# Optimization experiments

Measured on AMD Instinct MI355X. Metric: run time of the kernel, lower is better.

Reference implementation:

```python
import jax, jax.numpy as jnp
import numpy as np

TOP_K = 2  # matches init k


def setup_inputs() -> dict:
    key = jax.random.key(0)
    ks = jax.random.split(key, 5)
    B, S, D, E, H = 2, 2048, 1024, 8, 4096
    scale = 0.02
    return {
        "x": jax.random.normal(ks[0], (B, S, D), dtype=jnp.float32),
        "wg": jax.random.normal(ks[1], (D, E), dtype=jnp.float32) * scale,
        "w1": jax.random.normal(ks[2], (E, D, H), dtype=jnp.float32) * scale,
        "w3": jax.random.normal(ks[3], (E, D, H), dtype=jnp.float32) * scale,
        "w2": jax.random.normal(ks[4], (E, H, D), dtype=jnp.float32) * scale,
    }


def reference(x, wg, w1, w3, w2):
    # x: [B, S, D]; wg: [D, E]; w1/w3: [E, D, H]; w2: [E, H, D]
    B, S, D = x.shape
    E = wg.shape[1]
    T = B * S
    xt = x.reshape(T, D)

    # Top-k gating: softmax over expert logits, keep top-k, renormalize.
    logits = xt @ wg                                    # [T, E]
    probs = jax.nn.softmax(logits, axis=-1)             # [T, E]
    topv, topi = jax.lax.top_k(probs, TOP_K)            # [T, k]
    topv = topv / topv.sum(axis=-1, keepdims=True)
    # Dense combine weights [T, E] (zero for non-selected experts).
    comb = jnp.zeros((T, E), dtype=x.dtype).at[jnp.arange(T)[:, None], topi].set(topv)

    # Per-expert SwiGLU MLP with weighted combine (loop over small fixed E).
    out = jnp.zeros_like(xt)
    for e in range(E):
        h = jax.nn.silu(xt @ w1[e]) * (xt @ w3[e])      # [T, H]
        out = out + comb[:, e:e + 1] * (h @ w2[e])       # [T, D]
    return out.reshape(B, S, D)
```

## Files before the change

kernel.cpp:

```cpp
#include <hip/hip_runtime.h>
#include <cstdint>
#include <cstddef>

#define T_TOK 4096
#define DIM   1024
#define NEXP  8
#define HDIM  4096
#define NSLOT (2 * T_TOK)

#define BM 128
#define BN1 128
#define BN2 256
#define BK 32

typedef __attribute__((ext_vector_type(8))) short s16x8;
typedef __attribute__((ext_vector_type(4))) float f32x4;

__device__ __forceinline__ unsigned short f2bf(float f) {
    union { float f; unsigned u; } v; v.f = f;
    unsigned u = v.u;
    unsigned r = (u + 0x7FFFu + ((u >> 16) & 1u)) >> 16;
    return (unsigned short)r;
}

__device__ __forceinline__ int lds_off(int row, int kchunk) {
    return row * 32 + ((kchunk ^ ((row >> 1) & 3)) << 3);
}

__device__ __forceinline__ void gload16(const void* g, void* l) {
    __builtin_amdgcn_global_load_lds(
        (const __attribute__((address_space(1))) unsigned int*)g,
        (__attribute__((address_space(3))) unsigned int*)l, 16, 0, 0);
}

__global__ __launch_bounds__(256) void gate_kernel(
    const float* __restrict__ x, const float* __restrict__ wg,
    int* __restrict__ tok_e, float* __restrict__ tok_w, int* __restrict__ counts,
    unsigned short* __restrict__ xg)
{
    int t = blockIdx.x * 4 + (threadIdx.x >> 6);
    int lane = threadIdx.x & 63;
    float acc[NEXP];
#pragma unroll
    for (int e = 0; e < NEXP; ++e) acc[e] = 0.f;
    const float* xrow = x + (size_t)t * DIM;
    unsigned short* xgrow = xg + (size_t)t * DIM;
    for (int d = lane; d < DIM; d += 64) {
        float xv = xrow[d];
        xgrow[d] = f2bf(xv);
        const float4* wr = (const float4*)(wg + (size_t)d * NEXP);
        float4 w0 = wr[0], w1v = wr[1];
        acc[0] += xv * w0.x;  acc[1] += xv * w0.y;
        acc[2] += xv * w0.z;  acc[3] += xv * w0.w;
        acc[4] += xv * w1v.x; acc[5] += xv * w1v.y;
        acc[6] += xv * w1v.z; acc[7] += xv * w1v.w;
    }
#pragma unroll
    for (int e = 0; e < NEXP; ++e)
#pragma unroll
        for (int off = 32; off > 0; off >>= 1)
            acc[e] += __shfl_xor(acc[e], off);
    if (lane == 0) {
        int i0 = 0;
#pragma unroll
        for (int e = 1; e < NEXP; ++e) if (acc[e] > acc[i0]) i0 = e;
        int i1 = (i0 == 0) ? 1 : 0;
#pragma unroll
        for (int e = 0; e < NEXP; ++e) if (e != i0 && acc[e] > acc[i1]) i1 = e;
        float w0 = 1.f / (1.f + __expf(acc[i1] - acc[i0]));
        tok_e[2 * t] = i0;  tok_e[2 * t + 1] = i1;
        tok_w[2 * t] = w0;  tok_w[2 * t + 1] = 1.f - w0;
        atomicAdd(&counts[i0], 1);
        atomicAdd(&counts[i1], 1);
    }
}

__global__ void scan_kernel(const int* __restrict__ counts,
                            int* __restrict__ offsets, int* __restrict__ cursor)
{
    if (threadIdx.x == 0) {
        int s = 0;
        for (int e = 0; e < NEXP; ++e) { offsets[e] = s; s += counts[e]; cursor[e] = 0; }
        offsets[NEXP] = s;
    }
}

__global__ __launch_bounds__(256) void assign_kernel(
    const int* __restrict__ tok_e, const float* __restrict__ tok_w,
    const int* __restrict__ offsets, int* __restrict__ cursor,
    int* __restrict__ rows_tok, float* __restrict__ rows_gate)
{
    int t = blockIdx.x * 256 + threadIdx.x;
    if (t >= T_TOK) return;
#pragma unroll
    for (int j = 0; j < 2; ++j) {
        int e = tok_e[2 * t + j];
        int pos = offsets[e] + atomicAdd(&cursor[e], 1);
        rows_tok[pos] = t;
        rows_gate[pos] = tok_w[2 * t + j];
    }
}

__device__ __forceinline__ void tconv_body(
    const float* __restrict__ src, unsigned short* __restrict__ dst,
    int R, int C, int e, int bx, int by, int t)
{
    __shared__ unsigned int t_lds[64 * 33];
    int c0 = bx * 64, r0 = by * 64;
    int lane = t & 63, w = t >> 6;
    const float* s = src + (size_t)e * R * C + (size_t)(r0 + w * 16) * C + c0 + lane;
#pragma unroll
    for (int j = 0; j < 8; ++j) {
        float v0 = s[(size_t)(2 * j) * C];
        float v1 = s[(size_t)(2 * j + 1) * C];
        unsigned int pk = (unsigned int)f2bf(v0) | ((unsigned int)f2bf(v1) << 16);
        t_lds[lane * 33 + (w * 8 + j)] = pk;
    }
    __syncthreads();
    unsigned short* dbase = dst + (size_t)e * C * R;
#pragma unroll
    for (int rep = 0; rep < 2; ++rep) {
        int idx = rep * 256 + t;
        int c = idx >> 3, chunk = idx & 7;
        uint4 o;
        o.x = t_lds[c * 33 + chunk * 4 + 0];
        o.y = t_lds[c * 33 + chunk * 4 + 1];
        o.z = t_lds[c * 33 + chunk * 4 + 2];
        o.w = t_lds[c * 33 + chunk * 4 + 3];
        *(uint4*)(dbase + (size_t)(c0 + c) * R + r0 + chunk * 8) = o;
    }
}

__global__ __launch_bounds__(256) void tconv13_kernel(
    const float* __restrict__ w1, const float* __restrict__ w3,
    unsigned short* __restrict__ w1t, unsigned short* __restrict__ w3t)
{
    int z = blockIdx.z;
    if (z < NEXP)
        tconv_body(w1, w1t, DIM, HDIM, z, blockIdx.x, blockIdx.y, threadIdx.x);
    else
        tconv_body(w3, w3t, DIM, HDIM, z - NEXP, blockIdx.x, blockIdx.y, threadIdx.x);
}

__global__ __launch_bounds__(256) void tconv_kernel(
    const float* __restrict__ src, unsigned short* __restrict__ dst, int R, int C)
{
    tconv_body(src, dst, R, C, blockIdx.z, blockIdx.x, blockIdx.y, threadIdx.x);
}

__global__ __launch_bounds__(512, 4) void gemm1_kernel(
    const unsigned short* __restrict__ xg,
    const unsigned short* __restrict__ w1t, const unsigned short* __restrict__ w3t,
    const int* __restrict__ rows_tok, const int* __restrict__ offsets,
    unsigned short* __restrict__ h)
{
    int e = blockIdx.z;
    int offs = offsets[e];
    int cnt  = offsets[e + 1] - offs;
    int m0 = blockIdx.y * BM;
    if (m0 >= cnt) return;
    int n0 = blockIdx.x * BN1;

    __shared__ unsigned short lds3[3][3][BM * BK];
    __shared__ int toks[BM];

    int tid = threadIdx.x;
    if (tid < BM) toks[tid] = rows_tok[offs + min(m0 + tid, cnt - 1)];
    __syncthreads();

    int lane = tid & 63;
    int wid = tid >> 6;
    int wr = wid >> 2, wc = wid & 3;
    int lr = lane & 15, lg = lane >> 4;

    int srow = tid >> 2;
    int g = (tid & 3) ^ ((srow >> 1) & 3);
    const unsigned short* asrc  = xg  + (size_t)toks[srow] * DIM + g * 8;
    const unsigned short* b1src = w1t + ((size_t)e * HDIM + n0 + srow) * DIM + g * 8;
    const unsigned short* b3src = w3t + ((size_t)e * HDIM + n0 + srow) * DIM + g * 8;
    int ldsbase = wid * 512;

    f32x4 acc1[4][2] = {};
    f32x4 acc3[4][2] = {};

    const int NT = DIM / BK;

    auto stage_t = [&](int b, int t) {
        int k0 = t * BK;
        gload16(asrc + k0,  &lds3[b][0][ldsbase]);
        gload16(b1src + k0, &lds3[b][1][ldsbase]);
        gload16(b3src + k0, &lds3[b][2][ldsbase]);
    };

    stage_t(0, 0);
    stage_t(1, 1);

    int cur = 0;
    for (int t = 0; t < NT; ++t) {
        if (t == NT - 1) asm volatile("s_waitcnt vmcnt(0)" ::: "memory");
        else             asm volatile("s_waitcnt vmcnt(3)" ::: "memory");
        __builtin_amdgcn_s_barrier();

        int nxt = cur + 2; if (nxt >= 3) nxt -= 3;
        if (t + 2 < NT) stage_t(nxt, t + 2);

        s16x8 a[4], b1f[2], b3f[2];
#pragma unroll
        for (int m = 0; m < 4; ++m)
            a[m] = *(const s16x8*)&lds3[cur][0][lds_off(wr * 64 + m * 16 + lr, lg)];
#pragma unroll
        for (int n = 0; n < 2; ++n) {
            b1f[n] = *(const s16x8*)&lds3[cur][1][lds_off(wc * 32 + n * 16 + lr, lg)];
            b3f[n] = *(const s16x8*)&lds3[cur][2][lds_off(wc * 32 + n * 16 + lr, lg)];
        }

        __builtin_amdgcn_s_setprio(1);
#pragma unroll
        for (int n = 0; n < 2; ++n) {
#pragma unroll
            for (int m = 0; m < 4; ++m)
                acc1[m][n] = __builtin_amdgcn_mfma_f32_16x16x32_bf16(a[m], b1f[n], acc1[m][n], 0, 0, 0);
#pragma unroll
            for (int m = 0; m < 4; ++m)
                acc3[m][n] = __builtin_amdgcn_mfma_f32_16x16x32_bf16(a[m], b3f[n], acc3[m][n], 0, 0, 0);
        }
        __builtin_amdgcn_s_setprio(0);

        __builtin_amdgcn_s_barrier();
        cur = cur + 1; if (cur == 3) cur = 0;
    }

#pragma unroll
    for (int m = 0; m < 4; ++m)
#pragma unroll
        for (int n = 0; n < 2; ++n)
#pragma unroll
            for (int r = 0; r < 4; ++r) {
                int row_local = wr * 64 + m * 16 + lg * 4 + r;
                if (m0 + row_local < cnt) {
                    int col_local = wc * 32 + n * 16 + lr;
                    float g1 = acc1[m][n][r];
                    float hv = (g1 / (1.f + __expf(-g1))) * acc3[m][n][r];
                    h[(size_t)(offs + m0 + row_local) * HDIM + n0 + col_local] = f2bf(hv);
                }
            }
}

__global__ __launch_bounds__(512, 4) void gemm2_kernel(
    const unsigned short* __restrict__ h, const unsigned short* __restrict__ w2t,
    const int* __restrict__ rows_tok, const float* __restrict__ rows_gate,
    const int* __restrict__ offsets, float* __restrict__ out)
{
    int e = blockIdx.z;
    int offs = offsets[e];
    int cnt  = offsets[e + 1] - offs;
    int m0 = blockIdx.y * BM;
    if (m0 >= cnt) return;
    int n0 = blockIdx.x * BN2;

    __shared__ unsigned short ldsA[3][BM * BK];
    __shared__ unsigned short ldsB[3][BN2 * BK];
    __shared__ int   toks[BM];
    __shared__ float gts[BM];

    int tid = threadIdx.x;
    if (tid < BM) {
        int p = offs + min(m0 + tid, cnt - 1);
        toks[tid] = rows_tok[p];
        gts[tid]  = rows_gate[p];
    }
    __syncthreads();

    int lane = tid & 63;
    int wid = tid >> 6;
    int wr = wid >> 2, wc = wid & 3;
    int lr = lane & 15, lg = lane >> 4;

    int srow = tid >> 2;
    int g = (tid & 3) ^ ((srow >> 1) & 3);
    int arow = offs + min(m0 + srow, cnt - 1);
    const unsigned short* asrc  = h + (size_t)arow * HDIM + g * 8;
    const unsigned short* bsrc0 = w2t + ((size_t)e * DIM + n0 + srow) * HDIM + g * 8;
    const unsigned short* bsrc1 = w2t + ((size_t)e * DIM + n0 + 128 + srow) * HDIM + g * 8;
    int ldsbase = wid * 512;

    f32x4 acc[4][4] = {};

    const int NT = HDIM / BK;

    auto stage_t = [&](int b, int t) {
        int k0 = t * BK;
        gload16(asrc + k0,  &ldsA[b][ldsbase]);
        gload16(bsrc0 + k0, &ldsB[b][ldsbase]);
        gload16(bsrc1 + k0, &ldsB[b][4096 + ldsbase]);
    };

    stage_t(0, 0);
    stage_t(1, 1);

    int cur = 0;
    for (int t = 0; t < NT; ++t) {
        if (t == NT - 1) asm volatile("s_waitcnt vmcnt(0)" ::: "memory");
        else             asm volatile("s_waitcnt vmcnt(3)" ::: "memory");
        __builtin_amdgcn_s_barrier();

        int nxt = cur + 2; if (nxt >= 3) nxt -= 3;
        if (t + 2 < NT) stage_t(nxt, t + 2);

        s16x8 a[4], bf[4];
#pragma unroll
        for (int m = 0; m < 4; ++m)
            a[m] = *(const s16x8*)&ldsA[cur][lds_off(wr * 64 + m * 16 + lr, lg)];
#pragma unroll
        for (int n = 0; n < 4; ++n)
            bf[n] = *(const s16x8*)&ldsB[cur][lds_off(wc * 64 + n * 16 + lr, lg)];

        __builtin_amdgcn_s_setprio(1);
#pragma unroll
        for (int n = 0; n < 4; ++n)
#pragma unroll
            for (int m = 0; m < 4; ++m)
                acc[m][n] = __builtin_amdgcn_mfma_f32_16x16x32_bf16(a[m], bf[n], acc[m][n], 0, 0, 0);
        __builtin_amdgcn_s_setprio(0);

        __builtin_amdgcn_s_barrier();
        cur = cur + 1; if (cur == 3) cur = 0;
    }

#pragma unroll
    for (int m = 0; m < 4; ++m)
#pragma unroll
        for (int n = 0; n < 4; ++n)
#pragma unroll
            for (int r = 0; r < 4; ++r) {
                int row_local = wr * 64 + m * 16 + lg * 4 + r;
                if (m0 + row_local < cnt) {
                    int col = n0 + wc * 64 + n * 16 + lr;
                    float v = acc[m][n][r] * gts[row_local];
                    atomicAdd(&out[(size_t)toks[row_local] * DIM + col], v);
                }
            }
}

extern "C" void kernel_launch(void* const* d_in, const int* in_sizes, int n_in,
                              void* d_out, int out_size, void* d_ws, size_t ws_size,
                              hipStream_t stream)
{
    const float* x  = (const float*)d_in[0];
    const float* wg = (const float*)d_in[1];
    const float* w1 = (const float*)d_in[2];
    const float* w3 = (const float*)d_in[3];
    const float* w2 = (const float*)d_in[4];
    float* out = (float*)d_out;

    char* ws = (char*)d_ws;
    size_t off = 0;
    auto alloc = [&](size_t bytes) -> void* {
        void* p = ws + off;
        off = (off + bytes + 255) & ~(size_t)255;
        return p;
    };
    int*   rows_tok  = (int*)alloc((size_t)NSLOT * 4);
    float* rows_gate = (float*)alloc((size_t)NSLOT * 4);
    int*   tok_e     = (int*)alloc((size_t)NSLOT * 4);
    float* tok_w     = (float*)alloc((size_t)NSLOT * 4);
    int*   counts    = (int*)alloc(NEXP * 4);
    int*   offsets   = (int*)alloc((NEXP + 1) * 4);
    int*   cursor    = (int*)alloc(NEXP * 4);
    unsigned short* xg   = (unsigned short*)alloc((size_t)T_TOK * DIM * 2);
    unsigned short* w1t  = (unsigned short*)alloc((size_t)NEXP * HDIM * DIM * 2);
    unsigned short* w3t  = (unsigned short*)alloc((size_t)NEXP * HDIM * DIM * 2);
    unsigned short* hbuf = (unsigned short*)alloc((size_t)NSLOT * HDIM * 2);
    unsigned short* w2t  = w1t;

    hipMemsetAsync(counts, 0, NEXP * 4, stream);
    hipMemsetAsync(out, 0, (size_t)out_size * sizeof(float), stream);

    gate_kernel<<<T_TOK / 4, 256, 0, stream>>>(x, wg, tok_e, tok_w, counts, xg);
    scan_kernel<<<1, 64, 0, stream>>>(counts, offsets, cursor);
    assign_kernel<<<T_TOK / 256, 256, 0, stream>>>(tok_e, tok_w, offsets, cursor,
                                                   rows_tok, rows_gate);

    tconv13_kernel<<<dim3(HDIM / 64, DIM / 64, 2 * NEXP), 256, 0, stream>>>(
        w1, w3, w1t, w3t);

    gemm1_kernel<<<dim3(HDIM / BN1, T_TOK / BM, NEXP), 512, 0, stream>>>(
        xg, w1t, w3t, rows_tok, offsets, hbuf);

    tconv_kernel<<<dim3(DIM / 64, HDIM / 64, NEXP), 256, 0, stream>>>(w2, w2t, HDIM, DIM);

    gemm2_kernel<<<dim3(DIM / BN2, T_TOK / BM, NEXP), 512, 0, stream>>>(
        hbuf, w2t, rows_tok, rows_gate, offsets, out);
}
```

Measured before the change: 585.2 us.

## Interleave w1/w3 rows into one B matrix and pair gate/up via lane shuffle

The weight transpose kernel now writes w1 and w3 rows interleaved into a single buffer, so gemm1 loads one B tile instead of two. It keeps one accumulator set, and the SwiGLU pairing is done with a lane xor-shuffle in the epilogue. Columns per block are halved in effective output and the grid doubles in x. The cut in LDS and registers lets the launch bound occupancy rise from 4 to 6. In exchange, half the lanes are idle during the epilogue stores and the output writes become strided rather than contiguous.

```diff
diff --git a/kernel.cpp b/kernel.cpp
--- a/kernel.cpp
+++ b/kernel.cpp
@@ -131,15 +131,40 @@
     }
 }
 
-__global__ __launch_bounds__(256) void tconv13_kernel(
+__global__ __launch_bounds__(256) void tconv13i_kernel(
     const float* __restrict__ w1, const float* __restrict__ w3,
-    unsigned short* __restrict__ w1t, unsigned short* __restrict__ w3t)
-{
+    unsigned short* __restrict__ w13t)
+{
+    __shared__ unsigned int t_lds[64 * 33];
     int z = blockIdx.z;
-    if (z < NEXP)
-        tconv_body(w1, w1t, DIM, HDIM, z, blockIdx.x, blockIdx.y, threadIdx.x);
-    else
-        tconv_body(w3, w3t, DIM, HDIM, z - NEXP, blockIdx.x, blockIdx.y, threadIdx.x);
+    int parity = (z >= NEXP) ? 1 : 0;
+    int e = parity ? z - NEXP : z;
+    const float* src = parity ? w3 : w1;
+    const int R = DIM, C = HDIM;
+    int c0 = blockIdx.x * 64, r0 = blockIdx.y * 64;
+    int t = threadIdx.x;
+    int lane = t & 63, w = t >> 6;
+    const float* s = src + (size_t)e * R * C + (size_t)(r0 + w * 16) * C + c0 + lane;
+#pragma unroll
+    for (int j = 0; j < 8; ++j) {
+        float v0 = s[(size_t)(2 * j) * C];
+        float v1 = s[(size_t)(2 * j + 1) * C];
+        unsigned int pk = (unsigned int)f2bf(v0) | ((unsigned int)f2bf(v1) << 16);
+        t_lds[lane * 33 + (w * 8 + j)] = pk;
+    }
+    __syncthreads();
+    unsigned short* dbase = w13t + (size_t)e * 2 * C * R;
+#pragma unroll
+    for (int rep = 0; rep < 2; ++rep) {
+        int idx = rep * 256 + t;
+        int c = idx >> 3, chunk = idx & 7;
+        uint4 o;
+        o.x = t_lds[c * 33 + chunk * 4 + 0];
+        o.y = t_lds[c * 33 + chunk * 4 + 1];
+        o.z = t_lds[c * 33 + chunk * 4 + 2];
+        o.w = t_lds[c * 33 + chunk * 4 + 3];
+        *(uint4*)(dbase + (size_t)(2 * (c0 + c) + parity) * R + r0 + chunk * 8) = o;
+    }
 }
 
 __global__ __launch_bounds__(256) void tconv_kernel(
@@ -148,9 +173,9 @@
     tconv_body(src, dst, R, C, blockIdx.z, blockIdx.x, blockIdx.y, threadIdx.x);
 }
 
-__global__ __launch_bounds__(512, 4) void gemm1_kernel(
+__global__ __launch_bounds__(512, 6) void gemm1_kernel(
     const unsigned short* __restrict__ xg,
-    const unsigned short* __restrict__ w1t, const unsigned short* __restrict__ w3t,
+    const unsigned short* __restrict__ w13t,
     const int* __restrict__ rows_tok, const int* __restrict__ offsets,
     unsigned short* __restrict__ h)
 {
@@ -161,7 +186,7 @@
     if (m0 >= cnt) return;
     int n0 = blockIdx.x * BN1;
 
-    __shared__ unsigned short lds3[3][3][BM * BK];
+    __shared__ unsigned short lds3[3][2][BM * BK];
     __shared__ int toks[BM];
 
     int tid = threadIdx.x;
@@ -175,21 +200,18 @@
 
     int srow = tid >> 2;
     int g = (tid & 3) ^ ((srow >> 1) & 3);
-    const unsigned short* asrc  = xg  + (size_t)toks[srow] * DIM + g * 8;
-    const unsigned short* b1src = w1t + ((size_t)e * HDIM + n0 + srow) * DIM + g * 8;
-    const unsigned short* b3src = w3t + ((size_t)e * HDIM + n0 + srow) * DIM + g * 8;
+    const unsigned short* asrc = xg   + (size_t)toks[srow] * DIM + g * 8;
+    const unsigned short* bsrc = w13t + ((size_t)e * 2 * HDIM + n0 + srow) * DIM + g * 8;
     int ldsbase = wid * 512;
 
-    f32x4 acc1[4][2] = {};
-    f32x4 acc3[4][2] = {};
+    f32x4 acc[4][2] = {};
 
     const int NT = DIM / BK;
 
     auto stage_t = [&](int b, int t) {
         int k0 = t * BK;
-        gload16(asrc + k0,  &lds3[b][0][ldsbase]);
-        gload16(b1src + k0, &lds3[b][1][ldsbase]);
-        gload16(b3src + k0, &lds3[b][2][ldsbase]);
+        gload16(asrc + k0, &lds3[b][0][ldsbase]);
+        gload16(bsrc + k0, &lds3[b][1][ldsbase]);
     };
 
     stage_t(0, 0);
@@ -198,32 +220,26 @@
     int cur = 0;
     for (int t = 0; t < NT; ++t) {
         if (t == NT - 1) asm volatile("s_waitcnt vmcnt(0)" ::: "memory");
-        else             asm volatile("s_waitcnt vmcnt(3)" ::: "memory");
+        else             asm volatile("s_waitcnt vmcnt(2)" ::: "memory");
         __builtin_amdgcn_s_barrier();
 
         int nxt = cur + 2; if (nxt >= 3) nxt -= 3;
         if (t + 2 < NT) stage_t(nxt, t + 2);
 
-        s16x8 a[4], b1f[2], b3f[2];
+        s16x8 a[4], bf[2];
 #pragma unroll
         for (int m = 0; m < 4; ++m)
             a[m] = *(const s16x8*)&lds3[cur][0][lds_off(wr * 64 + m * 16 + lr, lg)];
 #pragma unroll
-        for (int n = 0; n < 2; ++n) {
-            b1f[n] = *(const s16x8*)&lds3[cur][1][lds_off(wc * 32 + n * 16 + lr, lg)];
-            b3f[n] = *(const s16x8*)&lds3[cur][2][lds_off(wc * 32 + n * 16 + lr, lg)];
-        }
+        for (int n = 0; n < 2; ++n)
+            bf[n] = *(const s16x8*)&lds3[cur][1][lds_off(wc * 32 + n * 16 + lr, lg)];
 
         __builtin_amdgcn_s_setprio(1);
 #pragma unroll
-        for (int n = 0; n < 2; ++n) {
+        for (int n = 0; n < 2; ++n)
 #pragma unroll
             for (int m = 0; m < 4; ++m)
-                acc1[m][n] = __builtin_amdgcn_mfma_f32_16x16x32_bf16(a[m], b1f[n], acc1[m][n], 0, 0, 0);
-#pragma unroll
-            for (int m = 0; m < 4; ++m)
-                acc3[m][n] = __builtin_amdgcn_mfma_f32_16x16x32_bf16(a[m], b3f[n], acc3[m][n], 0, 0, 0);
-        }
+                acc[m][n] = __builtin_amdgcn_mfma_f32_16x16x32_bf16(a[m], bf[n], acc[m][n], 0, 0, 0);
         __builtin_amdgcn_s_setprio(0);
 
         __builtin_amdgcn_s_barrier();
@@ -236,12 +252,14 @@
         for (int n = 0; n < 2; ++n)
 #pragma unroll
             for (int r = 0; r < 4; ++r) {
+                float g1 = acc[m][n][r];
+                float g3 = __shfl_xor(g1, 1);
                 int row_local = wr * 64 + m * 16 + lg * 4 + r;
-                if (m0 + row_local < cnt) {
-                    int col_local = wc * 32 + n * 16 + lr;
-                    float g1 = acc1[m][n][r];
-                    float hv = (g1 / (1.f + __expf(-g1))) * acc3[m][n][r];
-                    h[(size_t)(offs + m0 + row_local) * HDIM + n0 + col_local] = f2bf(hv);
+                if (((lane & 1) == 0) && (m0 + row_local < cnt)) {
+                    int gcol = n0 + wc * 32 + n * 16 + lr;
+                    int hcol = gcol >> 1;
+                    float hv = (g1 / (1.f + __expf(-g1))) * g3;
+                    h[(size_t)(offs + m0 + row_local) * HDIM + hcol] = f2bf(hv);
                 }
             }
 }
@@ -368,10 +386,9 @@
     int*   offsets   = (int*)alloc((NEXP + 1) * 4);
     int*   cursor    = (int*)alloc(NEXP * 4);
     unsigned short* xg   = (unsigned short*)alloc((size_t)T_TOK * DIM * 2);
-    unsigned short* w1t  = (unsigned short*)alloc((size_t)NEXP * HDIM * DIM * 2);
-    unsigned short* w3t  = (unsigned short*)alloc((size_t)NEXP * HDIM * DIM * 2);
+    unsigned short* w13t = (unsigned short*)alloc((size_t)NEXP * 2 * HDIM * DIM * 2);
     unsigned short* hbuf = (unsigned short*)alloc((size_t)NSLOT * HDIM * 2);
-    unsigned short* w2t  = w1t;
+    unsigned short* w2t  = w13t;
 
     hipMemsetAsync(counts, 0, NEXP * 4, stream);
     hipMemsetAsync(out, 0, (size_t)out_size * sizeof(float), stream);
@@ -381,11 +398,11 @@
     assign_kernel<<<T_TOK / 256, 256, 0, stream>>>(tok_e, tok_w, offsets, cursor,
                                                    rows_tok, rows_gate);
 
-    tconv13_kernel<<<dim3(HDIM / 64, DIM / 64, 2 * NEXP), 256, 0, stream>>>(
-        w1, w3, w1t, w3t);
-
-    gemm1_kernel<<<dim3(HDIM / BN1, T_TOK / BM, NEXP), 512, 0, stream>>>(
-        xg, w1t, w3t, rows_tok, offsets, hbuf);
+    tconv13i_kernel<<<dim3(HDIM / 64, DIM / 64, 2 * NEXP), 256, 0, stream>>>(
+        w1, w3, w13t);
+
+    gemm1_kernel<<<dim3(2 * HDIM / BN1, T_TOK / BM, NEXP), 512, 0, stream>>>(
+        xg, w13t, rows_tok, offsets, hbuf);
 
     tconv_kernel<<<dim3(DIM / 64, HDIM / 64, NEXP), 256, 0, stream>>>(w2, w2t, HDIM, DIM);
 
```

New measurement: 598.9 us. 1.02x slower.

## Load A operand directly from global into registers, shrink GEMM2 N tile

Applied to the files above, without the earlier changes.

Both grouped GEMMs stop staging the activation (A) tile through LDS. Each wave instead loads its A fragments straight from global memory into registers, double-buffered across even and odd k-steps, while only the weight tiles keep using the LDS triple buffer. GEMM2's N tile shrinks from 256 to 128, which halves its accumulators and doubles its grid. This removes LDS traffic and space for A and should raise occupancy, but adds uncoalesced per-lane global loads, duplicated A reads across the four waves that share rows, and extra reloads of the A rows in GEMM2.

```diff
diff --git a/kernel.cpp b/kernel.cpp
--- a/kernel.cpp
+++ b/kernel.cpp
@@ -10,7 +10,7 @@
 
 #define BM 128
 #define BN1 128
-#define BN2 256
+#define BN2 128
 #define BK 32
 
 typedef __attribute__((ext_vector_type(8))) short s16x8;
@@ -161,7 +161,7 @@
     if (m0 >= cnt) return;
     int n0 = blockIdx.x * BN1;
 
-    __shared__ unsigned short lds3[3][3][BM * BK];
+    __shared__ unsigned short lds3[3][2][BM * BK];
     __shared__ int toks[BM];
 
     int tid = threadIdx.x;
@@ -175,43 +175,46 @@
 
     int srow = tid >> 2;
     int g = (tid & 3) ^ ((srow >> 1) & 3);
-    const unsigned short* asrc  = xg  + (size_t)toks[srow] * DIM + g * 8;
     const unsigned short* b1src = w1t + ((size_t)e * HDIM + n0 + srow) * DIM + g * 8;
     const unsigned short* b3src = w3t + ((size_t)e * HDIM + n0 + srow) * DIM + g * 8;
     int ldsbase = wid * 512;
 
+    const unsigned short* abase[4];
+#pragma unroll
+    for (int m = 0; m < 4; ++m) {
+        int row = wr * 64 + m * 16 + lr;
+        abase[m] = xg + (size_t)toks[row] * DIM + lg * 8;
+    }
+
     f32x4 acc1[4][2] = {};
     f32x4 acc3[4][2] = {};
 
     const int NT = DIM / BK;
 
-    auto stage_t = [&](int b, int t) {
+    auto stageB = [&](int b, int t) {
         int k0 = t * BK;
-        gload16(asrc + k0,  &lds3[b][0][ldsbase]);
-        gload16(b1src + k0, &lds3[b][1][ldsbase]);
-        gload16(b3src + k0, &lds3[b][2][ldsbase]);
+        gload16(b1src + k0, &lds3[b][0][ldsbase]);
+        gload16(b3src + k0, &lds3[b][1][ldsbase]);
     };
 
-    stage_t(0, 0);
-    stage_t(1, 1);
-
-    int cur = 0;
-    for (int t = 0; t < NT; ++t) {
+    auto body = [&](int t, int cur, s16x8 (&au)[4], s16x8 (&ap)[4]) {
+        if (t + 1 < NT) {
+#pragma unroll
+            for (int m = 0; m < 4; ++m)
+                ap[m] = *(const s16x8*)(abase[m] + (t + 1) * BK);
+        }
         if (t == NT - 1) asm volatile("s_waitcnt vmcnt(0)" ::: "memory");
-        else             asm volatile("s_waitcnt vmcnt(3)" ::: "memory");
+        else             asm volatile("s_waitcnt vmcnt(6)" ::: "memory");
         __builtin_amdgcn_s_barrier();
 
         int nxt = cur + 2; if (nxt >= 3) nxt -= 3;
-        if (t + 2 < NT) stage_t(nxt, t + 2);
-
-        s16x8 a[4], b1f[2], b3f[2];
-#pragma unroll
-        for (int m = 0; m < 4; ++m)
-            a[m] = *(const s16x8*)&lds3[cur][0][lds_off(wr * 64 + m * 16 + lr, lg)];
+        if (t + 2 < NT) stageB(nxt, t + 2);
+
+        s16x8 b1f[2], b3f[2];
 #pragma unroll
         for (int n = 0; n < 2; ++n) {
-            b1f[n] = *(const s16x8*)&lds3[cur][1][lds_off(wc * 32 + n * 16 + lr, lg)];
-            b3f[n] = *(const s16x8*)&lds3[cur][2][lds_off(wc * 32 + n * 16 + lr, lg)];
+            b1f[n] = *(const s16x8*)&lds3[cur][0][lds_off(wc * 32 + n * 16 + lr, lg)];
+            b3f[n] = *(const s16x8*)&lds3[cur][1][lds_off(wc * 32 + n * 16 + lr, lg)];
         }
 
         __builtin_amdgcn_s_setprio(1);
@@ -219,15 +222,26 @@
         for (int n = 0; n < 2; ++n) {
 #pragma unroll
             for (int m = 0; m < 4; ++m)
-                acc1[m][n] = __builtin_amdgcn_mfma_f32_16x16x32_bf16(a[m], b1f[n], acc1[m][n], 0, 0, 0);
+                acc1[m][n] = __builtin_amdgcn_mfma_f32_16x16x32_bf16(au[m], b1f[n], acc1[m][n], 0, 0, 0);
 #pragma unroll
             for (int m = 0; m < 4; ++m)
-                acc3[m][n] = __builtin_amdgcn_mfma_f32_16x16x32_bf16(a[m], b3f[n], acc3[m][n], 0, 0, 0);
+                acc3[m][n] = __builtin_amdgcn_mfma_f32_16x16x32_bf16(au[m], b3f[n], acc3[m][n], 0, 0, 0);
         }
         __builtin_amdgcn_s_setprio(0);
-
         __builtin_amdgcn_s_barrier();
-        cur = cur + 1; if (cur == 3) cur = 0;
+    };
+
+    s16x8 aE[4], aO[4];
+#pragma unroll
+    for (int m = 0; m < 4; ++m) aE[m] = *(const s16x8*)(abase[m]);
+    stageB(0, 0);
+    stageB(1, 1);
+
+    int cur = 0;
+#pragma unroll 1
+    for (int t = 0; t < NT; t += 2) {
+        body(t, cur, aE, aO);      cur = (cur == 2) ? 0 : cur + 1;
+        body(t + 1, cur, aO, aE);  cur = (cur == 2) ? 0 : cur + 1;
     }
 
 #pragma unroll
@@ -258,7 +272,6 @@
     if (m0 >= cnt) return;
     int n0 = blockIdx.x * BN2;
 
-    __shared__ unsigned short ldsA[3][BM * BK];
     __shared__ unsigned short ldsB[3][BN2 * BK];
     __shared__ int   toks[BM];
     __shared__ float gts[BM];
@@ -278,64 +291,74 @@
 
     int srow = tid >> 2;
     int g = (tid & 3) ^ ((srow >> 1) & 3);
-    int arow = offs + min(m0 + srow, cnt - 1);
-    const unsigned short* asrc  = h + (size_t)arow * HDIM + g * 8;
-    const unsigned short* bsrc0 = w2t + ((size_t)e * DIM + n0 + srow) * HDIM + g * 8;
-    const unsigned short* bsrc1 = w2t + ((size_t)e * DIM + n0 + 128 + srow) * HDIM + g * 8;
+    const unsigned short* bsrc = w2t + ((size_t)e * DIM + n0 + srow) * HDIM + g * 8;
     int ldsbase = wid * 512;
 
-    f32x4 acc[4][4] = {};
+    const unsigned short* abase[4];
+#pragma unroll
+    for (int m = 0; m < 4; ++m) {
+        int row = offs + min(m0 + wr * 64 + m * 16 + lr, cnt - 1);
+        abase[m] = h + (size_t)row * HDIM + lg * 8;
+    }
+
+    f32x4 acc[4][2] = {};
 
     const int NT = HDIM / BK;
 
-    auto stage_t = [&](int b, int t) {
-        int k0 = t * BK;
-        gload16(asrc + k0,  &ldsA[b][ldsbase]);
-        gload16(bsrc0 + k0, &ldsB[b][ldsbase]);
-        gload16(bsrc1 + k0, &ldsB[b][4096 + ldsbase]);
+    auto stageB = [&](int b, int t) {
+        gload16(bsrc + t * BK, &ldsB[b][ldsbase]);
     };
 
-    stage_t(0, 0);
-    stage_t(1, 1);
+    auto body = [&](int t, int cur, s16x8 (&au)[4], s16x8 (&ap)[4]) {
+        if (t + 1 < NT) {
+#pragma unroll
+            for (int m = 0; m < 4; ++m)
+                ap[m] = *(const s16x8*)(abase[m] + (t + 1) * BK);
+        }
+        if (t == NT - 1) asm volatile("s_waitcnt vmcnt(0)" ::: "memory");
+        else             asm volatile("s_waitcnt vmcnt(5)" ::: "memory");
+        __builtin_amdgcn_s_barrier();
+
+        int nxt = cur + 2; if (nxt >= 3) nxt -= 3;
+        if (t + 2 < NT) stageB(nxt, t + 2);
+
+        s16x8 bf[2];
+#pragma unroll
+        for (int n = 0; n < 2; ++n)
+            bf[n] = *(const s16x8*)&ldsB[cur][lds_off(wc * 32 + n * 16 + lr, lg)];
+
+        __builtin_amdgcn_s_setprio(1);
+#pragma unroll
+        for (int n = 0; n < 2; ++n)
+#pragma unroll
+            for (int m = 0; m < 4; ++m)
+                acc[m][n] = __builtin_amdgcn_mfma_f32_16x16x32_bf16(au[m], bf[n], acc[m][n], 0, 0, 0);
+        __builtin_amdgcn_s_setprio(0);
+        __builtin_amdgcn_s_barrier();
+    };
+
+    s16x8 aE[4], aO[4];
+#pragma unroll
+    for (int m = 0; m < 4; ++m) aE[m] = *(const s16x8*)(abase[m]);
+    stageB(0, 0);
+    stageB(1, 1);
 
     int cur = 0;
-    for (int t = 0; t < NT; ++t) {
-        if (t == NT - 1) asm volatile("s_waitcnt vmcnt(0)" ::: "memory");
-        else             asm volatile("s_waitcnt vmcnt(3)" ::: "memory");
-        __builtin_amdgcn_s_barrier();
-
-        int nxt = cur + 2; if (nxt >= 3) nxt -= 3;
-        if (t + 2 < NT) stage_t(nxt, t + 2);
-
-        s16x8 a[4], bf[4];
-#pragma unroll
-        for (int m = 0; m < 4; ++m)
-            a[m] = *(const s16x8*)&ldsA[cur][lds_off(wr * 64 + m * 16 + lr, lg)];
-#pragma unroll
-        for (int n = 0; n < 4; ++n)
-            bf[n] = *(const s16x8*)&ldsB[cur][lds_off(wc * 64 + n * 16 + lr, lg)];
-
-        __builtin_amdgcn_s_setprio(1);
-#pragma unroll
-        for (int n = 0; n < 4; ++n)
-#pragma unroll
-            for (int m = 0; m < 4; ++m)
-                acc[m][n] = __builtin_amdgcn_mfma_f32_16x16x32_bf16(a[m], bf[n], acc[m][n], 0, 0, 0);
-        __builtin_amdgcn_s_setprio(0);
-
-        __builtin_amdgcn_s_barrier();
-        cur = cur + 1; if (cur == 3) cur = 0;
+#pragma unroll 1
+    for (int t = 0; t < NT; t += 2) {
+        body(t, cur, aE, aO);      cur = (cur == 2) ? 0 : cur + 1;
+        body(t + 1, cur, aO, aE);  cur = (cur == 2) ? 0 : cur + 1;
     }
 
 #pragma unroll
     for (int m = 0; m < 4; ++m)
 #pragma unroll
-        for (int n = 0; n < 4; ++n)
+        for (int n = 0; n < 2; ++n)
 #pragma unroll
             for (int r = 0; r < 4; ++r) {
                 int row_local = wr * 64 + m * 16 + lg * 4 + r;
                 if (m0 + row_local < cnt) {
-                    int col = n0 + wc * 64 + n * 16 + lr;
+                    int col = n0 + wc * 32 + n * 16 + lr;
                     float v = acc[m][n][r] * gts[row_local];
                     atomicAdd(&out[(size_t)toks[row_local] * DIM + col], v);
                 }
```

Result: slower. 1.116 ms (+90.6%).
